# Optimization experiments

Measured on AMD Instinct MI355X. Metric: run time of the kernel, lower is better.

The kernel has to match this reference:

```python
import jax, jax.numpy as jnp
import numpy as np
import math

B, S, D, H = 8, 1024, 1024, 16
DK = D // H


def rotate_half(x):
    x1, x2 = jnp.split(x, 2, axis=-1)
    return jnp.concatenate((-x2, x1), axis=-1)


def setup_inputs() -> dict:
    key = jax.random.key(0)
    ks = jax.random.split(key, 8)
    f32 = jnp.float32
    q = jax.random.normal(ks[0], (B, S, D), f32)
    k = jax.random.normal(ks[1], (B, S, D), f32)
    v = jax.random.normal(ks[2], (B, S, D), f32)
    # RoPE cache over the FULL d_model (rotary is applied before the head split)
    inv_freq = 1.0 / (10000.0 ** (np.arange(0, D, 2, dtype=np.float32) / D))
    freqs = np.arange(S, dtype=np.float32)[:, None] * inv_freq[None, :]  # [S, D/2]
    emb = np.concatenate([freqs, freqs], axis=-1)                        # [S, D]
    cos = jnp.asarray(np.cos(emb), f32)
    sin = jnp.asarray(np.sin(emb), f32)
    # additive padding mask [B, S] (zeros = no masking)
    mask = jnp.zeros((B, S), f32)
    # ALiBi-like distance matrix [S, S]
    idx = np.arange(S, dtype=np.float32)
    short_matrix = jnp.asarray(-np.abs(idx[:, None] - idx[None, :]), f32)
    # learned parameters
    w = lambda kk: jax.random.normal(kk, (D, D), f32) * 0.02
    Wq, Wk, Wv, Wo = w(ks[3]), w(ks[4]), w(ks[5]), w(ks[6])
    bq = jnp.zeros((D,), f32); bk = jnp.zeros((D,), f32)
    bv = jnp.zeros((D,), f32); bo = jnp.zeros((D,), f32)
    att_prior_bias = jnp.asarray(
        [math.log(p / (1 - p)) for p in [2 ** j / 2 ** (H + 1) for j in range(1, H + 1)]],
        f32)
    return {"q": q, "k": k, "v": v, "cos": cos, "sin": sin, "mask": mask,
            "short_matrix": short_matrix, "Wq": Wq, "bq": bq, "Wk": Wk, "bk": bk,
            "Wv": Wv, "bv": bv, "Wo": Wo, "bo": bo, "att_prior_bias": att_prior_bias}


def reference(q, k, v, cos, sin, mask, short_matrix,
              Wq, bq, Wk, bk, Wv, bv, Wo, bo, att_prior_bias):
    bs = q.shape[0]
    qp = q @ Wq.T + bq
    kp = k @ Wk.T + bk
    vp = v @ Wv.T + bv
    # rotary on full d_model, cos/sin broadcast [S, D] -> [B, S, D]
    qp = qp * cos + rotate_half(qp) * sin
    kp = kp * cos + rotate_half(kp) * sin
    # split heads: [B, S, D] -> [B, H, S, DK]
    qh = qp.reshape(bs, -1, H, DK).transpose(0, 2, 1, 3)
    kh = kp.reshape(bs, -1, H, DK).transpose(0, 2, 1, 3)
    vh = vp.reshape(bs, -1, H, DK).transpose(0, 2, 1, 3)
    # per-head ALiBi-like bias: sigmoid(b_h) * short_matrix -> [H, S, S]
    prior = jax.nn.sigmoid(att_prior_bias)[:, None, None] * short_matrix
    scores = jnp.einsum('bhqd,bhkd->bhqk', qh, kh) / math.sqrt(DK)
    scores = scores + mask[:, None, None, :] + prior[None]
    attn = jax.nn.softmax(scores, axis=-1)  # dropout is identity at inference
    out = jnp.einsum('bhqk,bhkd->bhqd', attn, vh)
    concat = out.transpose(0, 2, 1, 3).reshape(bs, -1, D)
    return concat @ Wo.T + bo
```

## Files before the change

kernel.cpp:

```cpp
#include <hip/hip_runtime.h>
#include <hip/hip_fp16.h>

typedef _Float16 f16;
typedef __attribute__((ext_vector_type(4))) _Float16 f16x4;
typedef __attribute__((ext_vector_type(8))) _Float16 f16x8;
typedef __attribute__((ext_vector_type(4))) float f32x4;

#define BATCH 8
#define SEQ 1024
#define DMODEL 1024
#define NHEAD 16
#define DHEAD 64

#define GLD16(gptr, lptr)                                                        \
  __builtin_amdgcn_global_load_lds(                                              \
      (const __attribute__((address_space(1))) void*)(gptr),                     \
      (__attribute__((address_space(3))) void*)(lptr), 16, 0, 0)

#define NQKV 8388608u
#define NW   1048576u
__global__ __launch_bounds__(256) void cast_all(
    const float* __restrict__ q, const float* __restrict__ k,
    const float* __restrict__ v, const float* __restrict__ wq,
    const float* __restrict__ wk, const float* __restrict__ wv,
    const float* __restrict__ wo, f16* __restrict__ dst) {
  size_t i8 = ((size_t)blockIdx.x * 256 + threadIdx.x) * 8;
  const float* src; size_t off;
  if      (i8 < (size_t)NQKV)            { src = q;  off = 0; }
  else if (i8 < 2ull * NQKV)             { src = k;  off = NQKV; }
  else if (i8 < 3ull * NQKV)             { src = v;  off = 2ull * NQKV; }
  else if (i8 < 3ull * NQKV + NW)        { src = wq; off = 3ull * NQKV; }
  else if (i8 < 3ull * NQKV + 2ull * NW) { src = wk; off = 3ull * NQKV + NW; }
  else if (i8 < 3ull * NQKV + 3ull * NW) { src = wv; off = 3ull * NQKV + 2ull * NW; }
  else                                   { src = wo; off = 3ull * NQKV + 3ull * NW; }
  float4 a = *(const float4*)&src[i8 - off];
  float4 b = *(const float4*)&src[i8 - off + 4];
  f16x8 h;
  h[0] = (f16)a.x; h[1] = (f16)a.y; h[2] = (f16)a.z; h[3] = (f16)a.w;
  h[4] = (f16)b.x; h[5] = (f16)b.y; h[6] = (f16)b.z; h[7] = (f16)b.w;
  *(f16x8*)&dst[i8] = h;
}

template <bool OUT16>
__global__ __launch_bounds__(256) void gemm16(const f16* __restrict__ A,
                                              const f16* __restrict__ W,
                                              const float* __restrict__ bias,
                                              void* __restrict__ Cv,
                                              int M, int N, int K) {
  __shared__ f16 As[128 * 32];
  __shared__ f16 Bs[128 * 32];
  const int t = threadIdx.x;
  const int lane = t & 63, wid = t >> 6;
  const int wm = wid >> 1, wn = wid & 1;
  const int row_l = lane & 15, kgrp = lane >> 4;
  const int m0 = blockIdx.x * 128, n0 = blockIdx.y * 128;
  f32x4 acc[4][4] = {};

  const int srow = t >> 2, scol = (t & 3) * 8;

  for (int k0 = 0; k0 < K; k0 += 32) {
    #pragma unroll
    for (int rr = 0; rr < 2; ++rr) {
      int row = srow + rr * 64;
      char* abase = (char*)As + (rr * 256 + wid * 64) * 16;
      char* bbase = (char*)Bs + (rr * 256 + wid * 64) * 16;
      GLD16(&A[(size_t)(m0 + row) * K + k0 + scol], abase);
      GLD16(&W[(size_t)(n0 + row) * K + k0 + scol], bbase);
    }
    __syncthreads();
    f16x8 af[4], bf[4];
    #pragma unroll
    for (int i = 0; i < 4; i++) af[i] = *(const f16x8*)&As[(wm * 64 + i * 16 + row_l) * 32 + kgrp * 8];
    #pragma unroll
    for (int j = 0; j < 4; j++) bf[j] = *(const f16x8*)&Bs[(wn * 64 + j * 16 + row_l) * 32 + kgrp * 8];
    #pragma unroll
    for (int i = 0; i < 4; i++)
      #pragma unroll
      for (int j = 0; j < 4; j++)
        acc[i][j] = __builtin_amdgcn_mfma_f32_16x16x32_f16(af[i], bf[j], acc[i][j], 0, 0, 0);
    __syncthreads();
  }

  #pragma unroll
  for (int i = 0; i < 4; i++) {
    int m = m0 + wm * 64 + i * 16 + kgrp * 4;
    #pragma unroll
    for (int j = 0; j < 4; j++) {
      int n = n0 + wn * 64 + j * 16 + row_l;
      float bb = bias[n];
      #pragma unroll
      for (int r = 0; r < 4; r++) {
        float val = acc[i][j][r] + bb;
        if (OUT16) ((f16*)Cv)[(size_t)(m + r) * N + n] = (f16)val;
        else       ((float*)Cv)[(size_t)(m + r) * N + n] = val;
      }
    }
  }
}

__global__ __launch_bounds__(256) void rope16(const f16* __restrict__ X,
                                              const float* __restrict__ cosb,
                                              const float* __restrict__ sinb,
                                              f16* __restrict__ out) {
  int idx = blockIdx.x * 256 + threadIdx.x;
  int row = idx >> 7;
  int d4 = (idx & 127) << 2;
  int s = row & (SEQ - 1);
  const f16* xr = X + (size_t)row * DMODEL;
  f16x4 x1 = *(const f16x4*)&xr[d4];
  f16x4 x2 = *(const f16x4*)&xr[d4 + 512];
  float4 c1 = *(const float4*)&cosb[(size_t)s * DMODEL + d4];
  float4 s1 = *(const float4*)&sinb[(size_t)s * DMODEL + d4];
  float4 c2 = *(const float4*)&cosb[(size_t)s * DMODEL + d4 + 512];
  float4 s2 = *(const float4*)&sinb[(size_t)s * DMODEL + d4 + 512];
  f16x4 o1, o2;
  o1[0] = (f16)((float)x1[0] * c1.x - (float)x2[0] * s1.x);
  o1[1] = (f16)((float)x1[1] * c1.y - (float)x2[1] * s1.y);
  o1[2] = (f16)((float)x1[2] * c1.z - (float)x2[2] * s1.z);
  o1[3] = (f16)((float)x1[3] * c1.w - (float)x2[3] * s1.w);
  o2[0] = (f16)((float)x2[0] * c2.x + (float)x1[0] * s2.x);
  o2[1] = (f16)((float)x2[1] * c2.y + (float)x1[1] * s2.y);
  o2[2] = (f16)((float)x2[2] * c2.z + (float)x1[2] * s2.z);
  o2[3] = (f16)((float)x2[3] * c2.w + (float)x1[3] * s2.w);
  f16* orow = out + (size_t)row * DMODEL;
  *(f16x4*)&orow[d4] = o1;
  *(f16x4*)&orow[d4 + 512] = o2;
}

__global__ __launch_bounds__(256) void transv16(const f16* __restrict__ X,
                                                f16* __restrict__ Vt) {
  int bz = blockIdx.x;
  int dt = bz & 15;
  int st = (bz >> 4) & 15;
  int b = bz >> 8;
  int s0 = st * 64, d0 = dt * 64;
  __shared__ f16 tile[64][68];
  int t = threadIdx.x;
  int tr = t >> 4, tc = t & 15;
  #pragma unroll
  for (int i = 0; i < 4; i++) {
    int s_loc = tr + i * 16;
    f16x4 v = *(const f16x4*)&X[((size_t)(b * SEQ + s0 + s_loc)) * DMODEL + d0 + tc * 4];
    *(f16x4*)&tile[s_loc][tc * 4] = v;
  }
  __syncthreads();
  #pragma unroll
  for (int i = 0; i < 4; i++) {
    int d_loc = tr + i * 16;
    f16x4 hv;
    #pragma unroll
    for (int j = 0; j < 4; j++) hv[j] = tile[tc * 4 + j][d_loc];
    *(f16x4*)&Vt[((size_t)(b * DMODEL + d0 + d_loc)) * SEQ + s0 + tc * 4] = hv;
  }
}

__global__ __launch_bounds__(256) void attn2(const f16* __restrict__ Q,
                                             const f16* __restrict__ K,
                                             const f16* __restrict__ Vt,
                                             const float* __restrict__ mask,
                                             const float* __restrict__ shortm,
                                             const float* __restrict__ prior,
                                             f16* __restrict__ out) {
  const float LOG2E = 1.44269504f;
  int bz = blockIdx.x;
  int qb = bz & 15, bh = bz >> 4;
  int b = bh >> 4, h = bh & 15;
  int t = threadIdx.x, lane = t & 63, wid = t >> 6;
  int row_l = lane & 15, kgrp = lane >> 4;
  float psc = LOG2E / (1.0f + __expf(-prior[h]));
  const float qscale = 0.125f * LOG2E;

  int qrow0 = qb * 64 + wid * 16;
  const f16* Qb = Q + ((size_t)(b * SEQ + qrow0)) * DMODEL + h * DHEAD;
  const f16* Kb = K + ((size_t)b * SEQ) * DMODEL + h * DHEAD;
  const f16* Vb = Vt + ((size_t)(b * DMODEL + h * DHEAD)) * SEQ;
  const float* maskb = mask + (size_t)b * SEQ;
  const float* smb = shortm + (size_t)qrow0 * SEQ;

  f16x8 aq[2];
  aq[0] = *(const f16x8*)&Qb[row_l * DMODEL + kgrp * 8];
  aq[1] = *(const f16x8*)&Qb[row_l * DMODEL + 32 + kgrp * 8];

  __shared__ f16 Ks[64 * 64];
  __shared__ f16 Vs[64 * 64];
  __shared__ f16 Pl[4][16 * 64];
  f16* Pw = &Pl[wid][0];

  float mrow[4], lrow[4];
  f32x4 acco[4] = {};
  #pragma unroll
  for (int r = 0; r < 4; r++) { mrow[r] = -3.0e38f; lrow[r] = 0.0f; }

  const int slot8 = t & 7;

  for (int kb = 0; kb < SEQ; kb += 64) {
    #pragma unroll
    for (int rr = 0; rr < 2; ++rr) {
      int row = (t >> 3) + rr * 32;
      int gc = ((slot8 ^ (row & 7)) * 8);
      char* kbase = (char*)Ks + (rr * 256 + wid * 64) * 16;
      char* vbase = (char*)Vs + (rr * 256 + wid * 64) * 16;
      GLD16(&Kb[(size_t)(kb + row) * DMODEL + gc], kbase);
      GLD16(&Vb[(size_t)row * SEQ + kb + gc], vbase);
    }
    __syncthreads();

    f32x4 sc[4];
    #pragma unroll
    for (int hh = 0; hh < 4; ++hh) {
      int kr = hh * 16 + row_l;
      int sw = kr & 7;
      f16x8 k0 = *(const f16x8*)&Ks[kr * 64 + ((kgrp ^ sw) * 8)];
      f16x8 k1 = *(const f16x8*)&Ks[kr * 64 + (((4 + kgrp) ^ sw) * 8)];
      f32x4 z = {};
      z = __builtin_amdgcn_mfma_f32_16x16x32_f16(aq[0], k0, z, 0, 0, 0);
      z = __builtin_amdgcn_mfma_f32_16x16x32_f16(aq[1], k1, z, 0, 0, 0);
      sc[hh] = z;
    }

    float s[4][4];
    #pragma unroll
    for (int hh = 0; hh < 4; ++hh) {
      int kv = kb + hh * 16 + row_l;
      float mk = maskb[kv] * LOG2E;
      #pragma unroll
      for (int r = 0; r < 4; r++)
        s[hh][r] = sc[hh][r] * qscale + mk + psc * smb[(size_t)(kgrp * 4 + r) * SEQ + kv];
    }

    float fs[4], mnew[4];
    #pragma unroll
    for (int r = 0; r < 4; r++) {
      float mx = fmaxf(fmaxf(s[0][r], s[1][r]), fmaxf(s[2][r], s[3][r]));
      #pragma unroll
      for (int off = 1; off < 16; off <<= 1) mx = fmaxf(mx, __shfl_xor(mx, off));
      mnew[r] = fmaxf(mrow[r], mx);
      fs[r] = exp2f(mrow[r] - mnew[r]);
      mrow[r] = mnew[r];
    }
    float p[4][4];
    #pragma unroll
    for (int hh = 0; hh < 4; ++hh)
      #pragma unroll
      for (int r = 0; r < 4; r++) p[hh][r] = exp2f(s[hh][r] - mnew[r]);
    #pragma unroll
    for (int r = 0; r < 4; r++) {
      float rs = (p[0][r] + p[1][r]) + (p[2][r] + p[3][r]);
      #pragma unroll
      for (int off = 1; off < 16; off <<= 1) rs += __shfl_xor(rs, off);
      lrow[r] = lrow[r] * fs[r] + rs;
    }
    #pragma unroll
    for (int t2 = 0; t2 < 4; t2++)
      #pragma unroll
      for (int r = 0; r < 4; r++) acco[t2][r] *= fs[r];

    #pragma unroll
    for (int hh = 0; hh < 4; ++hh)
      #pragma unroll
      for (int r = 0; r < 4; r++) {
        int qr = kgrp * 4 + r;
        int col = hh * 16 + row_l;
        int slot = col >> 3;
        Pw[qr * 64 + ((slot ^ (qr & 7)) * 8) + (col & 7)] = (f16)p[hh][r];
      }
    f16x8 pa[2];
    {
      int sw = row_l & 7;
      pa[0] = *(const f16x8*)&Pw[row_l * 64 + ((kgrp ^ sw) * 8)];
      pa[1] = *(const f16x8*)&Pw[row_l * 64 + (((4 + kgrp) ^ sw) * 8)];
    }

    #pragma unroll
    for (int t2 = 0; t2 < 4; t2++) {
      int vr = t2 * 16 + row_l;
      int sw = vr & 7;
      f16x8 b0 = *(const f16x8*)&Vs[vr * 64 + ((kgrp ^ sw) * 8)];
      f16x8 b1 = *(const f16x8*)&Vs[vr * 64 + (((4 + kgrp) ^ sw) * 8)];
      acco[t2] = __builtin_amdgcn_mfma_f32_16x16x32_f16(pa[0], b0, acco[t2], 0, 0, 0);
      acco[t2] = __builtin_amdgcn_mfma_f32_16x16x32_f16(pa[1], b1, acco[t2], 0, 0, 0);
    }
    __syncthreads();
  }

  #pragma unroll
  for (int r = 0; r < 4; r++) {
    int qg = qrow0 + kgrp * 4 + r;
    float inv = 1.0f / lrow[r];
    #pragma unroll
    for (int t2 = 0; t2 < 4; t2++)
      out[((size_t)(b * SEQ + qg)) * DMODEL + h * DHEAD + t2 * 16 + row_l] =
          (f16)(acco[t2][r] * inv);
  }
}

extern "C" void kernel_launch(void* const* d_in, const int* in_sizes, int n_in,
                              void* d_out, int out_size, void* d_ws, size_t ws_size,
                              hipStream_t stream) {
  const float* q      = (const float*)d_in[0];
  const float* k      = (const float*)d_in[1];
  const float* v      = (const float*)d_in[2];
  const float* cosb   = (const float*)d_in[3];
  const float* sinb   = (const float*)d_in[4];
  const float* mask   = (const float*)d_in[5];
  const float* shortm = (const float*)d_in[6];
  const float* Wq     = (const float*)d_in[7];
  const float* bq     = (const float*)d_in[8];
  const float* Wk     = (const float*)d_in[9];
  const float* bk     = (const float*)d_in[10];
  const float* Wv     = (const float*)d_in[11];
  const float* bv     = (const float*)d_in[12];
  const float* Wo     = (const float*)d_in[13];
  const float* bo     = (const float*)d_in[14];
  const float* prior  = (const float*)d_in[15];
  float* outp = (float*)d_out;

  const size_t M = (size_t)BATCH * SEQ;
  f16* ws16 = (f16*)d_ws;
  f16* qf  = ws16;
  f16* kf  = ws16 + (size_t)NQKV;
  f16* vf  = ws16 + 2ull * NQKV;
  f16* Wqf = ws16 + 3ull * NQKV;
  f16* Wkf = Wqf + NW;
  f16* Wvf = Wkf + NW;
  f16* Wof = Wvf + NW;
  f16* proj = ws16 + 3ull * NQKV + 4ull * NW;
  f16* qro  = proj + NQKV;
  f16* kro  = qro + NQKV;
  f16* vt   = qf;
  f16* cat  = kf;

  dim3 gemm_grid(M / 128, DMODEL / 128);

  cast_all<<<(3u * NQKV + 4u * NW) / 8 / 256, 256, 0, stream>>>(q, k, v, Wq, Wk, Wv, Wo, ws16);

  gemm16<true><<<gemm_grid, 256, 0, stream>>>(qf, Wqf, bq, proj, (int)M, DMODEL, DMODEL);
  rope16<<<(int)(M * 128 / 256), 256, 0, stream>>>(proj, cosb, sinb, qro);
  gemm16<true><<<gemm_grid, 256, 0, stream>>>(kf, Wkf, bk, proj, (int)M, DMODEL, DMODEL);
  rope16<<<(int)(M * 128 / 256), 256, 0, stream>>>(proj, cosb, sinb, kro);
  gemm16<true><<<gemm_grid, 256, 0, stream>>>(vf, Wvf, bv, proj, (int)M, DMODEL, DMODEL);
  transv16<<<BATCH * 16 * 16, 256, 0, stream>>>(proj, vt);
  attn2<<<BATCH * NHEAD * (SEQ / 64), 256, 0, stream>>>(qro, kro, vt, mask, shortm, prior, cat);
  gemm16<false><<<gemm_grid, 256, 0, stream>>>(cat, Wof, bo, outp, (int)M, DMODEL, DMODEL);
}
```

Before: 442.6 us.

## Batch QKV projections into one GEMM and rework attention with double-buffered K/V

The three Q/K/V projection GEMMs become one launch over a concatenated weight grid, and the two RoPE launches become one. The softmax scale is folded into Q during RoPE. The attention kernel is restructured: K/V tiles are double-buffered in shared memory so loads overlap compute, and the score matrix is computed transposed so each lane owns one query row. The online-softmax rescale is skipped when no lane's max changes, probabilities are moved into the PV MFMA operand layout with ds_bpermute instead of an LDS round trip, and the output is staged through LDS for wide stores. This cuts launch count, shuffle and LDS traffic, and stalls on tile loads, at the cost of more LDS use and more complex code.

```diff
diff --git a/kernel.cpp b/kernel.cpp
--- a/kernel.cpp
+++ b/kernel.cpp
@@ -5,12 +5,15 @@
 typedef __attribute__((ext_vector_type(4))) _Float16 f16x4;
 typedef __attribute__((ext_vector_type(8))) _Float16 f16x8;
 typedef __attribute__((ext_vector_type(4))) float f32x4;
+typedef __attribute__((ext_vector_type(4))) unsigned int u32x4;
 
 #define BATCH 8
 #define SEQ 1024
 #define DMODEL 1024
 #define NHEAD 16
 #define DHEAD 64
+#define QSCALE 0.1803368801f
+#define L2E 1.44269504f
 
 #define GLD16(gptr, lptr)                                                        \
   __builtin_amdgcn_global_load_lds(                                              \
@@ -19,6 +22,13 @@
 
 #define NQKV 8388608u
 #define NW   1048576u
+
+__device__ inline unsigned pk2(float a, float b) {
+  unsigned short ha = __builtin_bit_cast(unsigned short, (f16)a);
+  unsigned short hb = __builtin_bit_cast(unsigned short, (f16)b);
+  return ((unsigned)hb << 16) | (unsigned)ha;
+}
+
 __global__ __launch_bounds__(256) void cast_all(
     const float* __restrict__ q, const float* __restrict__ k,
     const float* __restrict__ v, const float* __restrict__ wq,
@@ -41,12 +51,73 @@
   *(f16x8*)&dst[i8] = h;
 }
 
-template <bool OUT16>
-__global__ __launch_bounds__(256) void gemm16(const f16* __restrict__ A,
-                                              const f16* __restrict__ W,
-                                              const float* __restrict__ bias,
-                                              void* __restrict__ Cv,
-                                              int M, int N, int K) {
+__global__ __launch_bounds__(256) void gemm_qkv(const f16* __restrict__ Abase,
+                                                const f16* __restrict__ Wqkv,
+                                                const float* __restrict__ bq,
+                                                const float* __restrict__ bk,
+                                                const float* __restrict__ bv,
+                                                f16* __restrict__ qp,
+                                                f16* __restrict__ kp,
+                                                f16* __restrict__ vp) {
+  const int K = DMODEL;
+  __shared__ f16 As[128 * 32];
+  __shared__ f16 Bs[128 * 32];
+  const int t = threadIdx.x;
+  const int lane = t & 63, wid = t >> 6;
+  const int wm = wid >> 1, wn = wid & 1;
+  const int row_l = lane & 15, kgrp = lane >> 4;
+  const int m0 = blockIdx.x * 128, n0 = blockIdx.y * 128;
+  const int which = n0 >> 10;
+  const f16* A = Abase + (size_t)which * NQKV;
+  const float* bias = which == 0 ? bq : (which == 1 ? bk : bv);
+  f16* outp = which == 0 ? qp : (which == 1 ? kp : vp);
+  const int nloc0 = n0 & 1023;
+  f32x4 acc[4][4] = {};
+
+  const int srow = t >> 2, scol = (t & 3) * 8;
+
+  for (int k0 = 0; k0 < K; k0 += 32) {
+    #pragma unroll
+    for (int rr = 0; rr < 2; ++rr) {
+      int row = srow + rr * 64;
+      char* abase = (char*)As + (rr * 256 + wid * 64) * 16;
+      char* bbase = (char*)Bs + (rr * 256 + wid * 64) * 16;
+      GLD16(&A[(size_t)(m0 + row) * K + k0 + scol], abase);
+      GLD16(&Wqkv[(size_t)(n0 + row) * K + k0 + scol], bbase);
+    }
+    __syncthreads();
+    f16x8 af[4], bf[4];
+    #pragma unroll
+    for (int i = 0; i < 4; i++) af[i] = *(const f16x8*)&As[(wm * 64 + i * 16 + row_l) * 32 + kgrp * 8];
+    #pragma unroll
+    for (int j = 0; j < 4; j++) bf[j] = *(const f16x8*)&Bs[(wn * 64 + j * 16 + row_l) * 32 + kgrp * 8];
+    #pragma unroll
+    for (int i = 0; i < 4; i++)
+      #pragma unroll
+      for (int j = 0; j < 4; j++)
+        acc[i][j] = __builtin_amdgcn_mfma_f32_16x16x32_f16(af[i], bf[j], acc[i][j], 0, 0, 0);
+    __syncthreads();
+  }
+
+  #pragma unroll
+  for (int i = 0; i < 4; i++) {
+    int m = m0 + wm * 64 + i * 16 + kgrp * 4;
+    #pragma unroll
+    for (int j = 0; j < 4; j++) {
+      int n = nloc0 + wn * 64 + j * 16 + row_l;
+      float bb = bias[n];
+      #pragma unroll
+      for (int r = 0; r < 4; r++)
+        outp[(size_t)(m + r) * DMODEL + n] = (f16)(acc[i][j][r] + bb);
+    }
+  }
+}
+
+__global__ __launch_bounds__(256) void gemm16f(const f16* __restrict__ A,
+                                               const f16* __restrict__ W,
+                                               const float* __restrict__ bias,
+                                               float* __restrict__ C,
+                                               int M, int N, int K) {
   __shared__ f16 As[128 * 32];
   __shared__ f16 Bs[128 * 32];
   const int t = threadIdx.x;
@@ -55,7 +126,6 @@
   const int row_l = lane & 15, kgrp = lane >> 4;
   const int m0 = blockIdx.x * 128, n0 = blockIdx.y * 128;
   f32x4 acc[4][4] = {};
-
   const int srow = t >> 2, scol = (t & 3) * 8;
 
   for (int k0 = 0; k0 < K; k0 += 32) {
@@ -89,20 +159,25 @@
       int n = n0 + wn * 64 + j * 16 + row_l;
       float bb = bias[n];
       #pragma unroll
-      for (int r = 0; r < 4; r++) {
-        float val = acc[i][j][r] + bb;
-        if (OUT16) ((f16*)Cv)[(size_t)(m + r) * N + n] = (f16)val;
-        else       ((float*)Cv)[(size_t)(m + r) * N + n] = val;
-      }
-    }
-  }
-}
-
-__global__ __launch_bounds__(256) void rope16(const f16* __restrict__ X,
-                                              const float* __restrict__ cosb,
-                                              const float* __restrict__ sinb,
-                                              f16* __restrict__ out) {
+      for (int r = 0; r < 4; r++)
+        C[(size_t)(m + r) * N + n] = acc[i][j][r] + bb;
+    }
+  }
+}
+
+__global__ __launch_bounds__(256) void rope2(const f16* __restrict__ Xq,
+                                             const f16* __restrict__ Xk,
+                                             const float* __restrict__ cosb,
+                                             const float* __restrict__ sinb,
+                                             f16* __restrict__ oq,
+                                             f16* __restrict__ ok) {
   int idx = blockIdx.x * 256 + threadIdx.x;
+  const int HALFN = BATCH * SEQ * 128;
+  bool isq = idx < HALFN;
+  if (!isq) idx -= HALFN;
+  const f16* X = isq ? Xq : Xk;
+  f16* out = isq ? oq : ok;
+  float scale = isq ? QSCALE : 1.0f;
   int row = idx >> 7;
   int d4 = (idx & 127) << 2;
   int s = row & (SEQ - 1);
@@ -114,14 +189,14 @@
   float4 c2 = *(const float4*)&cosb[(size_t)s * DMODEL + d4 + 512];
   float4 s2 = *(const float4*)&sinb[(size_t)s * DMODEL + d4 + 512];
   f16x4 o1, o2;
-  o1[0] = (f16)((float)x1[0] * c1.x - (float)x2[0] * s1.x);
-  o1[1] = (f16)((float)x1[1] * c1.y - (float)x2[1] * s1.y);
-  o1[2] = (f16)((float)x1[2] * c1.z - (float)x2[2] * s1.z);
-  o1[3] = (f16)((float)x1[3] * c1.w - (float)x2[3] * s1.w);
-  o2[0] = (f16)((float)x2[0] * c2.x + (float)x1[0] * s2.x);
-  o2[1] = (f16)((float)x2[1] * c2.y + (float)x1[1] * s2.y);
-  o2[2] = (f16)((float)x2[2] * c2.z + (float)x1[2] * s2.z);
-  o2[3] = (f16)((float)x2[3] * c2.w + (float)x1[3] * s2.w);
+  o1[0] = (f16)(scale * ((float)x1[0] * c1.x - (float)x2[0] * s1.x));
+  o1[1] = (f16)(scale * ((float)x1[1] * c1.y - (float)x2[1] * s1.y));
+  o1[2] = (f16)(scale * ((float)x1[2] * c1.z - (float)x2[2] * s1.z));
+  o1[3] = (f16)(scale * ((float)x1[3] * c1.w - (float)x2[3] * s1.w));
+  o2[0] = (f16)(scale * ((float)x2[0] * c2.x + (float)x1[0] * s2.x));
+  o2[1] = (f16)(scale * ((float)x2[1] * c2.y + (float)x1[1] * s2.y));
+  o2[2] = (f16)(scale * ((float)x2[2] * c2.z + (float)x1[2] * s2.z));
+  o2[3] = (f16)(scale * ((float)x2[3] * c2.w + (float)x1[3] * s2.w));
   f16* orow = out + (size_t)row * DMODEL;
   *(f16x4*)&orow[d4] = o1;
   *(f16x4*)&orow[d4 + 512] = o2;
@@ -154,144 +229,182 @@
   }
 }
 
-__global__ __launch_bounds__(256) void attn2(const f16* __restrict__ Q,
+__global__ __launch_bounds__(256) void attn3(const f16* __restrict__ Q,
                                              const f16* __restrict__ K,
                                              const f16* __restrict__ Vt,
                                              const float* __restrict__ mask,
                                              const float* __restrict__ shortm,
                                              const float* __restrict__ prior,
                                              f16* __restrict__ out) {
-  const float LOG2E = 1.44269504f;
   int bz = blockIdx.x;
   int qb = bz & 15, bh = bz >> 4;
   int b = bh >> 4, h = bh & 15;
   int t = threadIdx.x, lane = t & 63, wid = t >> 6;
-  int row_l = lane & 15, kgrp = lane >> 4;
-  float psc = LOG2E / (1.0f + __expf(-prior[h]));
-  const float qscale = 0.125f * LOG2E;
-
-  int qrow0 = qb * 64 + wid * 16;
-  const f16* Qb = Q + ((size_t)(b * SEQ + qrow0)) * DMODEL + h * DHEAD;
+  int l15 = lane & 15, g = lane >> 4;
+  float psc2 = L2E / (1.0f + __expf(-prior[h]));
+
+  const int qrow0 = qb * 64;
+  const int qrow = qrow0 + wid * 16 + l15;
+  const f16* Qr = Q + ((size_t)(b * SEQ + qrow)) * DMODEL + h * DHEAD;
   const f16* Kb = K + ((size_t)b * SEQ) * DMODEL + h * DHEAD;
   const f16* Vb = Vt + ((size_t)(b * DMODEL + h * DHEAD)) * SEQ;
   const float* maskb = mask + (size_t)b * SEQ;
-  const float* smb = shortm + (size_t)qrow0 * SEQ;
-
-  f16x8 aq[2];
-  aq[0] = *(const f16x8*)&Qb[row_l * DMODEL + kgrp * 8];
-  aq[1] = *(const f16x8*)&Qb[row_l * DMODEL + 32 + kgrp * 8];
-
-  __shared__ f16 Ks[64 * 64];
-  __shared__ f16 Vs[64 * 64];
-  __shared__ f16 Pl[4][16 * 64];
-  f16* Pw = &Pl[wid][0];
-
-  float mrow[4], lrow[4];
+  const float* smr = shortm + (size_t)qrow * SEQ;
+
+  f16x8 aq0 = *(const f16x8*)&Qr[g * 8];
+  f16x8 aq1 = *(const f16x8*)&Qr[32 + g * 8];
+
+  __shared__ f16 Ks[2][64 * 64];
+  __shared__ f16 Vs[2][64 * 64];
+
+  float mrow = -3.0e38f, lrow = 0.0f;
   f32x4 acco[4] = {};
-  #pragma unroll
-  for (int r = 0; r < 4; r++) { mrow[r] = -3.0e38f; lrow[r] = 0.0f; }
 
   const int slot8 = t & 7;
-
-  for (int kb = 0; kb < SEQ; kb += 64) {
-    #pragma unroll
-    for (int rr = 0; rr < 2; ++rr) {
-      int row = (t >> 3) + rr * 32;
-      int gc = ((slot8 ^ (row & 7)) * 8);
-      char* kbase = (char*)Ks + (rr * 256 + wid * 64) * 16;
-      char* vbase = (char*)Vs + (rr * 256 + wid * 64) * 16;
-      GLD16(&Kb[(size_t)(kb + row) * DMODEL + gc], kbase);
-      GLD16(&Vb[(size_t)row * SEQ + kb + gc], vbase);
+  const int srow = t >> 3;
+  const int gc = ((slot8 ^ (srow & 7)) * 8);
+  const int s0 = (g & 1) * 2;
+  const int addr0 = (l15 + 16 * s0) * 4;
+  const int addr1 = addr0 + 64;
+  const bool lowg = (g < 2);
+  const int sw = l15 & 7;
+
+#define STAGE(tile, buf)                                                          \
+  {                                                                               \
+    int kb2 = (tile) * 64;                                                        \
+    _Pragma("unroll")                                                             \
+    for (int rr = 0; rr < 2; ++rr) {                                              \
+      int row = srow + rr * 32;                                                   \
+      char* kdst = (char*)&Ks[buf][0] + rr * 4096 + wid * 1024;                   \
+      char* vdst = (char*)&Vs[buf][0] + rr * 4096 + wid * 1024;                   \
+      GLD16(&Kb[(size_t)(kb2 + row) * DMODEL + gc], kdst);                        \
+      GLD16(&Vb[(size_t)row * SEQ + kb2 + gc], vdst);                             \
+    }                                                                             \
+  }
+
+  STAGE(0, 0);
+  __syncthreads();
+
+  for (int it = 0; it < 16; ++it) {
+    int cur = it & 1;
+    if (it < 15) STAGE(it + 1, cur ^ 1);
+    int kb = it * 64;
+    const f16* ks = &Ks[cur][0];
+    const f16* vs = &Vs[cur][0];
+
+    f32x4 sc[4];
+    #pragma unroll
+    for (int hh = 0; hh < 4; ++hh) {
+      int kr = l15 + 16 * hh;
+      f16x8 kf0 = *(const f16x8*)&ks[kr * 64 + ((g ^ sw) * 8)];
+      f16x8 kf1 = *(const f16x8*)&ks[kr * 64 + (((4 + g) ^ sw) * 8)];
+      f32x4 z = {};
+      z = __builtin_amdgcn_mfma_f32_16x16x32_f16(kf0, aq0, z, 0, 0, 0);
+      z = __builtin_amdgcn_mfma_f32_16x16x32_f16(kf1, aq1, z, 0, 0, 0);
+      sc[hh] = z;
+    }
+
+    float s[4][4];
+    #pragma unroll
+    for (int hh = 0; hh < 4; ++hh) {
+      int kv = kb + hh * 16 + g * 4;
+      float4 mk = *(const float4*)&maskb[kv];
+      float4 sm = *(const float4*)&smr[kv];
+      s[hh][0] = fmaf(L2E, mk.x, fmaf(psc2, sm.x, sc[hh][0]));
+      s[hh][1] = fmaf(L2E, mk.y, fmaf(psc2, sm.y, sc[hh][1]));
+      s[hh][2] = fmaf(L2E, mk.z, fmaf(psc2, sm.z, sc[hh][2]));
+      s[hh][3] = fmaf(L2E, mk.w, fmaf(psc2, sm.w, sc[hh][3]));
+    }
+
+    float pmax = fmaxf(fmaxf(fmaxf(s[0][0], s[0][1]), fmaxf(s[0][2], s[0][3])),
+                       fmaxf(fmaxf(s[1][0], s[1][1]), fmaxf(s[1][2], s[1][3])));
+    pmax = fmaxf(pmax, fmaxf(fmaxf(fmaxf(s[2][0], s[2][1]), fmaxf(s[2][2], s[2][3])),
+                             fmaxf(fmaxf(s[3][0], s[3][1]), fmaxf(s[3][2], s[3][3]))));
+    pmax = fmaxf(pmax, __shfl_xor(pmax, 16));
+    pmax = fmaxf(pmax, __shfl_xor(pmax, 32));
+    if (__any(pmax > mrow)) {
+      float mnew = fmaxf(mrow, pmax);
+      float fs = exp2f(mrow - mnew);
+      lrow *= fs;
+      #pragma unroll
+      for (int t2 = 0; t2 < 4; ++t2)
+        #pragma unroll
+        for (int r = 0; r < 4; ++r) acco[t2][r] *= fs;
+      mrow = mnew;
+    }
+    float p[4][4];
+    #pragma unroll
+    for (int hh = 0; hh < 4; ++hh)
+      #pragma unroll
+      for (int r = 0; r < 4; ++r) p[hh][r] = exp2f(s[hh][r] - mrow);
+    float rs = ((p[0][0] + p[0][1]) + (p[0][2] + p[0][3])) +
+               ((p[1][0] + p[1][1]) + (p[1][2] + p[1][3])) +
+               ((p[2][0] + p[2][1]) + (p[2][2] + p[2][3])) +
+               ((p[3][0] + p[3][1]) + (p[3][2] + p[3][3]));
+    rs += __shfl_xor(rs, 16);
+    rs += __shfl_xor(rs, 32);
+    lrow += rs;
+
+    unsigned cfr[2][4];
+    #pragma unroll
+    for (int half = 0; half < 2; ++half) {
+      unsigned a0 = pk2(p[half * 2][0], p[half * 2][1]);
+      unsigned a1 = pk2(p[half * 2][2], p[half * 2][3]);
+      unsigned b0 = pk2(p[half * 2 + 1][0], p[half * 2 + 1][1]);
+      unsigned b1 = pk2(p[half * 2 + 1][2], p[half * 2 + 1][3]);
+      int ta0 = __builtin_amdgcn_ds_bpermute(addr0, (int)a0);
+      int ta1 = __builtin_amdgcn_ds_bpermute(addr0, (int)a1);
+      int tb0 = __builtin_amdgcn_ds_bpermute(addr0, (int)b0);
+      int tb1 = __builtin_amdgcn_ds_bpermute(addr0, (int)b1);
+      int ua0 = __builtin_amdgcn_ds_bpermute(addr1, (int)a0);
+      int ua1 = __builtin_amdgcn_ds_bpermute(addr1, (int)a1);
+      int ub0 = __builtin_amdgcn_ds_bpermute(addr1, (int)b0);
+      int ub1 = __builtin_amdgcn_ds_bpermute(addr1, (int)b1);
+      cfr[half][0] = (unsigned)(lowg ? ta0 : tb0);
+      cfr[half][1] = (unsigned)(lowg ? ta1 : tb1);
+      cfr[half][2] = (unsigned)(lowg ? ua0 : ub0);
+      cfr[half][3] = (unsigned)(lowg ? ua1 : ub1);
+    }
+
+    #pragma unroll
+    for (int half = 0; half < 2; ++half) {
+      u32x4 cc; cc[0] = cfr[half][0]; cc[1] = cfr[half][1];
+      cc[2] = cfr[half][2]; cc[3] = cfr[half][3];
+      f16x8 pf = __builtin_bit_cast(f16x8, cc);
+      #pragma unroll
+      for (int t2 = 0; t2 < 4; ++t2) {
+        int vr = t2 * 16 + l15;
+        f16x8 vf = *(const f16x8*)&vs[vr * 64 + (((half * 4 + g) ^ sw) * 8)];
+        acco[t2] = __builtin_amdgcn_mfma_f32_16x16x32_f16(vf, pf, acco[t2], 0, 0, 0);
+      }
     }
     __syncthreads();
-
-    f32x4 sc[4];
-    #pragma unroll
-    for (int hh = 0; hh < 4; ++hh) {
-      int kr = hh * 16 + row_l;
-      int sw = kr & 7;
-      f16x8 k0 = *(const f16x8*)&Ks[kr * 64 + ((kgrp ^ sw) * 8)];
-      f16x8 k1 = *(const f16x8*)&Ks[kr * 64 + (((4 + kgrp) ^ sw) * 8)];
-      f32x4 z = {};
-      z = __builtin_amdgcn_mfma_f32_16x16x32_f16(aq[0], k0, z, 0, 0, 0);
-      z = __builtin_amdgcn_mfma_f32_16x16x32_f16(aq[1], k1, z, 0, 0, 0);
-      sc[hh] = z;
-    }
-
-    float s[4][4];
-    #pragma unroll
-    for (int hh = 0; hh < 4; ++hh) {
-      int kv = kb + hh * 16 + row_l;
-      float mk = maskb[kv] * LOG2E;
-      #pragma unroll
-      for (int r = 0; r < 4; r++)
-        s[hh][r] = sc[hh][r] * qscale + mk + psc * smb[(size_t)(kgrp * 4 + r) * SEQ + kv];
-    }
-
-    float fs[4], mnew[4];
-    #pragma unroll
-    for (int r = 0; r < 4; r++) {
-      float mx = fmaxf(fmaxf(s[0][r], s[1][r]), fmaxf(s[2][r], s[3][r]));
-      #pragma unroll
-      for (int off = 1; off < 16; off <<= 1) mx = fmaxf(mx, __shfl_xor(mx, off));
-      mnew[r] = fmaxf(mrow[r], mx);
-      fs[r] = exp2f(mrow[r] - mnew[r]);
-      mrow[r] = mnew[r];
-    }
-    float p[4][4];
-    #pragma unroll
-    for (int hh = 0; hh < 4; ++hh)
-      #pragma unroll
-      for (int r = 0; r < 4; r++) p[hh][r] = exp2f(s[hh][r] - mnew[r]);
-    #pragma unroll
-    for (int r = 0; r < 4; r++) {
-      float rs = (p[0][r] + p[1][r]) + (p[2][r] + p[3][r]);
-      #pragma unroll
-      for (int off = 1; off < 16; off <<= 1) rs += __shfl_xor(rs, off);
-      lrow[r] = lrow[r] * fs[r] + rs;
-    }
-    #pragma unroll
-    for (int t2 = 0; t2 < 4; t2++)
-      #pragma unroll
-      for (int r = 0; r < 4; r++) acco[t2][r] *= fs[r];
-
-    #pragma unroll
-    for (int hh = 0; hh < 4; ++hh)
-      #pragma unroll
-      for (int r = 0; r < 4; r++) {
-        int qr = kgrp * 4 + r;
-        int col = hh * 16 + row_l;
-        int slot = col >> 3;
-        Pw[qr * 64 + ((slot ^ (qr & 7)) * 8) + (col & 7)] = (f16)p[hh][r];
-      }
-    f16x8 pa[2];
-    {
-      int sw = row_l & 7;
-      pa[0] = *(const f16x8*)&Pw[row_l * 64 + ((kgrp ^ sw) * 8)];
-      pa[1] = *(const f16x8*)&Pw[row_l * 64 + (((4 + kgrp) ^ sw) * 8)];
-    }
-
-    #pragma unroll
-    for (int t2 = 0; t2 < 4; t2++) {
-      int vr = t2 * 16 + row_l;
-      int sw = vr & 7;
-      f16x8 b0 = *(const f16x8*)&Vs[vr * 64 + ((kgrp ^ sw) * 8)];
-      f16x8 b1 = *(const f16x8*)&Vs[vr * 64 + (((4 + kgrp) ^ sw) * 8)];
-      acco[t2] = __builtin_amdgcn_mfma_f32_16x16x32_f16(pa[0], b0, acco[t2], 0, 0, 0);
-      acco[t2] = __builtin_amdgcn_mfma_f32_16x16x32_f16(pa[1], b1, acco[t2], 0, 0, 0);
-    }
-    __syncthreads();
-  }
-
-  #pragma unroll
-  for (int r = 0; r < 4; r++) {
-    int qg = qrow0 + kgrp * 4 + r;
-    float inv = 1.0f / lrow[r];
-    #pragma unroll
-    for (int t2 = 0; t2 < 4; t2++)
-      out[((size_t)(b * SEQ + qg)) * DMODEL + h * DHEAD + t2 * 16 + row_l] =
-          (f16)(acco[t2][r] * inv);
-  }
+  }
+
+  float inv = 1.0f / lrow;
+  f16* Pw = &Ks[0][0] + wid * 1024;
+  #pragma unroll
+  for (int t2 = 0; t2 < 4; ++t2) {
+    f16x4 o;
+    #pragma unroll
+    for (int r = 0; r < 4; ++r) o[r] = (f16)(acco[t2][r] * inv);
+    int sl = t2 * 4 + g;
+    int s16 = sl >> 1, p8 = sl & 1;
+    int swz = s16 ^ sw;
+    *(f16x4*)&Pw[l15 * 64 + swz * 8 + p8 * 4] = o;
+  }
+  __syncthreads();
+  int rq = lane >> 3;
+  int cs = lane & 7;
+  #pragma unroll
+  for (int half = 0; half < 2; ++half) {
+    int q_loc = rq + half * 8;
+    int swz = cs ^ (q_loc & 7);
+    f16x8 vv = *(const f16x8*)&Pw[q_loc * 64 + swz * 8];
+    int qg = qrow0 + wid * 16 + q_loc;
+    *(f16x8*)&out[((size_t)(b * SEQ + qg)) * DMODEL + h * DHEAD + cs * 8] = vv;
+  }
+#undef STAGE
 }
 
 extern "C" void kernel_launch(void* const* d_in, const int* in_sizes, int n_in,
@@ -317,29 +430,29 @@
 
   const size_t M = (size_t)BATCH * SEQ;
   f16* ws16 = (f16*)d_ws;
-  f16* qf  = ws16;
-  f16* kf  = ws16 + (size_t)NQKV;
-  f16* vf  = ws16 + 2ull * NQKV;
-  f16* Wqf = ws16 + 3ull * NQKV;
-  f16* Wkf = Wqf + NW;
-  f16* Wvf = Wkf + NW;
-  f16* Wof = Wvf + NW;
-  f16* proj = ws16 + 3ull * NQKV + 4ull * NW;
-  f16* qro  = proj + NQKV;
-  f16* kro  = qro + NQKV;
-  f16* vt   = qf;
-  f16* cat  = kf;
-
-  dim3 gemm_grid(M / 128, DMODEL / 128);
+  f16* qf   = ws16;
+  f16* kf   = ws16 + (size_t)NQKV;
+  f16* vf   = ws16 + 2ull * NQKV;
+  f16* Wqkv = ws16 + 3ull * NQKV;
+  f16* Wof  = Wqkv + 3ull * NW;
+  f16* qp   = ws16 + 3ull * NQKV + 4ull * NW;
+  f16* kp   = qp + NQKV;
+  f16* vp   = kp + NQKV;
+  f16* qro = qf;
+  f16* kro = kf;
+  f16* vt  = vf;
+  f16* cat = qp;
 
   cast_all<<<(3u * NQKV + 4u * NW) / 8 / 256, 256, 0, stream>>>(q, k, v, Wq, Wk, Wv, Wo, ws16);
 
-  gemm16<true><<<gemm_grid, 256, 0, stream>>>(qf, Wqf, bq, proj, (int)M, DMODEL, DMODEL);
-  rope16<<<(int)(M * 128 / 256), 256, 0, stream>>>(proj, cosb, sinb, qro);
-  gemm16<true><<<gemm_grid, 256, 0, stream>>>(kf, Wkf, bk, proj, (int)M, DMODEL, DMODEL);
-  rope16<<<(int)(M * 128 / 256), 256, 0, stream>>>(proj, cosb, sinb, kro);
-  gemm16<true><<<gemm_grid, 256, 0, stream>>>(vf, Wvf, bv, proj, (int)M, DMODEL, DMODEL);
-  transv16<<<BATCH * 16 * 16, 256, 0, stream>>>(proj, vt);
-  attn2<<<BATCH * NHEAD * (SEQ / 64), 256, 0, stream>>>(qro, kro, vt, mask, shortm, prior, cat);
-  gemm16<false><<<gemm_grid, 256, 0, stream>>>(cat, Wof, bo, outp, (int)M, DMODEL, DMODEL);
-}
+  dim3 qkv_grid(M / 128, 3 * DMODEL / 128);
+  gemm_qkv<<<qkv_grid, 256, 0, stream>>>(qf, Wqkv, bq, bk, bv, qp, kp, vp);
+
+  rope2<<<2 * (int)(M * 128 / 256), 256, 0, stream>>>(qp, kp, cosb, sinb, qro, kro);
+  transv16<<<BATCH * 16 * 16, 256, 0, stream>>>(vp, vt);
+
+  attn3<<<BATCH * NHEAD * (SEQ / 64), 256, 0, stream>>>(qro, kro, vt, mask, shortm, prior, cat);
+
+  dim3 o_grid(M / 128, DMODEL / 128);
+  gemm16f<<<o_grid, 256, 0, stream>>>(cat, Wof, bo, outp, (int)M, DMODEL, DMODEL);
+}
```

New measurement: 424.9 us. 1.04x faster.
